# Optimization experiments

Measured on AMD Instinct MI355X. Metric: run time of the kernel, lower is better.

Reference implementation:

```python
import jax, jax.numpy as jnp
import numpy as np

N = 100000   # nodes
E = 1600000  # edges per relation (avg in-degree 16)
D = 128      # gcn_hidden (in_feat == out_feat)
R = 2        # relations: forward_edge, backward_edge


def setup_inputs() -> dict:
    key = jax.random.key(0)
    ks = jax.random.split(key, 8)
    x = jax.random.normal(ks[0], (N, D), dtype=jnp.float32)
    src_fwd = jax.random.randint(ks[1], (E,), 0, N, dtype=jnp.int32)
    dst_fwd = jax.random.randint(ks[2], (E,), 0, N, dtype=jnp.int32)
    src_bwd = jax.random.randint(ks[3], (E,), 0, N, dtype=jnp.int32)
    dst_bwd = jax.random.randint(ks[4], (E,), 0, N, dtype=jnp.int32)
    # xavier_uniform with relu gain sqrt(2)
    gain = np.sqrt(2.0)
    lim_rel = gain * np.sqrt(6.0 / (D + D))
    rel_weight = jax.random.uniform(ks[5], (R, D, D), minval=-lim_rel, maxval=lim_rel, dtype=jnp.float32)
    loop_weight = jax.random.uniform(ks[6], (D, D), minval=-lim_rel, maxval=lim_rel, dtype=jnp.float32)
    h_bias = jnp.zeros((D,), dtype=jnp.float32)
    return {
        'x': x,
        'src_fwd': src_fwd, 'dst_fwd': dst_fwd,
        'src_bwd': src_bwd, 'dst_bwd': dst_bwd,
        'rel_weight': rel_weight, 'loop_weight': loop_weight, 'h_bias': h_bias,
    }


def _rel_conv(x, src, dst, W):
    # dgl GraphConv(norm='right', weight per relation): scatter-sum src feats to
    # dst, divide by clamped in-degree, then matmul W (in_feat == out_feat so
    # order of matmul vs aggregation is mathematically equivalent).
    msg = x[src]                                            # [E, D] gather
    agg = jax.ops.segment_sum(msg, dst, num_segments=N)     # [N, D] scatter-add
    deg = jax.ops.segment_sum(jnp.ones((src.shape[0],), x.dtype), dst, num_segments=N)
    agg = agg / jnp.clip(deg, 1.0)[:, None]                 # right norm, deg clamp(min=1)
    return agg @ W                                          # [N, D]


def reference(x, src_fwd, dst_fwd, src_bwd, dst_bwd, rel_weight, loop_weight, h_bias):
    h = _rel_conv(x, src_fwd, dst_fwd, rel_weight[0])
    h = h + _rel_conv(x, src_bwd, dst_bwd, rel_weight[1])   # HeteroGraphConv sums per-relation results
    h = h + x @ loop_weight                                 # self loop
    h = h + h_bias                                          # bias
    h = jax.nn.relu(h)                                      # activation
    return h                                                # dropout is identity in eval
```

## Files before the change

### kernel.cpp

```cpp
#include <hip/hip_runtime.h>
#include <hip/hip_bf16.h>


#define DFEAT 128
#define CH2 16384
#define NBMAX 1600
#define CAP 3328

typedef __attribute__((ext_vector_type(8))) short short8v;
typedef __attribute__((ext_vector_type(4))) float float4v;

__global__ void convert_kernel(const float4* __restrict__ x4,
                               ushort4* __restrict__ xb4, int n4) {
    int i = blockIdx.x * blockDim.x + threadIdx.x;
    if (i >= n4) return;
    float4 v = x4[i];
    ushort4 o;
    o.x = __hip_bfloat16_raw(__float2bfloat16(v.x)).x;
    o.y = __hip_bfloat16_raw(__float2bfloat16(v.y)).x;
    o.z = __hip_bfloat16_raw(__float2bfloat16(v.z)).x;
    o.w = __hip_bfloat16_raw(__float2bfloat16(v.w)).x;
    xb4[i] = o;
}

__global__ void pack_b_kernel(const float* __restrict__ wrel,
                              const float* __restrict__ wloop,
                              unsigned short* __restrict__ wb) {
    int t = blockIdx.x * blockDim.x + threadIdx.x;
    if (t >= 12 * 8 * 64) return;
    int lane = t & 63;
    int kbase = (t >> 9) * 32 + (lane >> 4) * 8;
    int col = (((t >> 6) & 7) << 4) + (lane & 15);
    unsigned short tmp[8];
#pragma unroll
    for (int j = 0; j < 8; ++j) {
        int k = kbase + j;
        float v = (k < 256) ? wrel[k * DFEAT + col] : wloop[(k - 256) * DFEAT + col];
        tmp[j] = __hip_bfloat16_raw(__float2bfloat16(v)).x;
    }
    *(ushort4*)(wb + t * 8)     = make_ushort4(tmp[0], tmp[1], tmp[2], tmp[3]);
    *(ushort4*)(wb + t * 8 + 4) = make_ushort4(tmp[4], tmp[5], tmp[6], tmp[7]);
}

__global__ void zero_kernel(int* __restrict__ p, int n) {
    int i = blockIdx.x * blockDim.x + threadIdx.x;
    if (i < n) p[i] = 0;
}

__global__ __launch_bounds__(256) void hist_kernel(
        const int* __restrict__ dst0, const int* __restrict__ dst1,
        int* __restrict__ ghist, int N, int E, int NB) {
    __shared__ int h[NBMAX];
    int tid = threadIdx.x;
    for (int i = tid; i < NBMAX; i += 256) h[i] = 0;
    __syncthreads();
    int lo = blockIdx.x * CH2, hi = min(2 * E, lo + CH2);
    for (int i = lo + tid; i < hi; i += 256) {
        int r = (i >= E) ? 1 : 0;
        int e = i - r * E;
        int t = r ? dst1[e] : dst0[e];
        atomicAdd(&h[(r * N + t) >> 7], 1);
    }
    __syncthreads();
    for (int b = tid; b < NB; b += 256) {
        int c = h[b];
        if (c) atomicAdd(&ghist[b], c);
    }
}

__global__ __launch_bounds__(256) void scan_kernel(const int* __restrict__ ghist,
                                                   int* __restrict__ S,
                                                   int* __restrict__ cursor,
                                                   int n, int total) {
    __shared__ int psum[256];
    int t = threadIdx.x;
    int cs = (n + 255) / 256;
    int s = 0;
    for (int j = 0; j < cs; ++j) {
        int idx = t * cs + j;
        if (idx < n) s += ghist[idx];
    }
    psum[t] = s; __syncthreads();
    for (int off = 1; off < 256; off <<= 1) {
        int add = (t >= off) ? psum[t - off] : 0;
        __syncthreads();
        psum[t] += add;
        __syncthreads();
    }
    int run = psum[t] - s;
    for (int j = 0; j < cs; ++j) {
        int idx = t * cs + j;
        if (idx < n) { S[idx] = run; cursor[idx] = run; run += ghist[idx]; }
    }
    if (t == 0) S[n] = total;
}

__global__ __launch_bounds__(256) void bin_kernel(
        const int* __restrict__ src0, const int* __restrict__ dst0,
        const int* __restrict__ src1, const int* __restrict__ dst1,
        int* __restrict__ cursor, unsigned* __restrict__ binned, int N, int E) {
    __shared__ int cnt[NBMAX];
    __shared__ int base[NBMAX];
    int tid = threadIdx.x;
    for (int i = tid; i < NBMAX; i += 256) cnt[i] = 0;
    __syncthreads();
    int lo = blockIdx.x * CH2, hi = min(2 * E, lo + CH2);
    for (int i = lo + tid; i < hi; i += 256) {
        int r = (i >= E) ? 1 : 0;
        int e = i - r * E;
        int t = r ? dst1[e] : dst0[e];
        atomicAdd(&cnt[(r * N + t) >> 7], 1);
    }
    __syncthreads();
    for (int b = tid; b < NBMAX; b += 256) {
        int c = cnt[b];
        if (c) base[b] = atomicAdd(&cursor[b], c);
    }
    __syncthreads();
    for (int i = lo + tid; i < hi; i += 256) {
        int r = (i >= E) ? 1 : 0;
        int e = i - r * E;
        int s = r ? src1[e] : src0[e];
        int t = r ? dst1[e] : dst0[e];
        int p = r * N + t;
        int slot = atomicAdd(&base[p >> 7], 1);
        binned[slot] = ((unsigned)(p & 127) << 17) | (unsigned)s;
    }
}

__global__ __launch_bounds__(256) void agg_kernel(
        const uint2* __restrict__ xb2,
        const unsigned* __restrict__ binned,
        const int* __restrict__ S,
        unsigned short* __restrict__ aggb, int M) {
    __shared__ unsigned ebuf[CAP];
    __shared__ int cnt[128], cur[128], rs[128], sh[128];
    int tid = threadIdx.x;
    int b = blockIdx.x;
    int estart = S[b], eend = S[b + 1];
    int total = eend - estart;
    int P0 = b << 7;
    int hw = tid >> 5, lane = tid & 31;

    if (total <= CAP) {
        if (tid < 128) cnt[tid] = 0;
        __syncthreads();
        for (int i = estart + tid; i < eend; i += 256)
            atomicAdd(&cnt[binned[i] >> 17], 1);
        __syncthreads();
        if (tid < 128) sh[tid] = cnt[tid];
        __syncthreads();
        for (int off = 1; off < 128; off <<= 1) {
            int add = (tid < 128 && tid >= off) ? sh[tid - off] : 0;
            __syncthreads();
            if (tid < 128) sh[tid] += add;
            __syncthreads();
        }
        if (tid < 128) { rs[tid] = sh[tid] - cnt[tid]; cur[tid] = sh[tid] - cnt[tid]; }
        __syncthreads();
        for (int i = estart + tid; i < eend; i += 256) {
            unsigned v = binned[i];
            int slot = atomicAdd(&cur[v >> 17], 1);
            ebuf[slot] = v;
        }
        __syncthreads();

        for (int pi = 0; pi < 16; ++pi) {
            int pl = hw * 16 + pi;
            int s0 = rs[pl], c = cnt[pl];
            float a0 = 0.f, a1 = 0.f, a2 = 0.f, a3 = 0.f;
            int e = 0;
            for (; e + 4 <= c; e += 4) {
                int sA = ebuf[s0 + e] & 0x1FFFF;
                int sB = ebuf[s0 + e + 1] & 0x1FFFF;
                int sC = ebuf[s0 + e + 2] & 0x1FFFF;
                int sD = ebuf[s0 + e + 3] & 0x1FFFF;
                uint2 gA = xb2[(long long)sA * 32 + lane];
                uint2 gB = xb2[(long long)sB * 32 + lane];
                uint2 gC = xb2[(long long)sC * 32 + lane];
                uint2 gD = xb2[(long long)sD * 32 + lane];
                a0 += __uint_as_float(gA.x << 16) + __uint_as_float(gB.x << 16)
                    + __uint_as_float(gC.x << 16) + __uint_as_float(gD.x << 16);
                a1 += __uint_as_float(gA.x & 0xffff0000u) + __uint_as_float(gB.x & 0xffff0000u)
                    + __uint_as_float(gC.x & 0xffff0000u) + __uint_as_float(gD.x & 0xffff0000u);
                a2 += __uint_as_float(gA.y << 16) + __uint_as_float(gB.y << 16)
                    + __uint_as_float(gC.y << 16) + __uint_as_float(gD.y << 16);
                a3 += __uint_as_float(gA.y & 0xffff0000u) + __uint_as_float(gB.y & 0xffff0000u)
                    + __uint_as_float(gC.y & 0xffff0000u) + __uint_as_float(gD.y & 0xffff0000u);
            }
            for (; e < c; ++e) {
                int s = ebuf[s0 + e] & 0x1FFFF;
                uint2 g = xb2[(long long)s * 32 + lane];
                a0 += __uint_as_float(g.x << 16);
                a1 += __uint_as_float(g.x & 0xffff0000u);
                a2 += __uint_as_float(g.y << 16);
                a3 += __uint_as_float(g.y & 0xffff0000u);
            }
            int pg = P0 + pl;
            if (pg < M) {
                float inv = 1.0f / (float)max(c, 1);
                ushort4 w;
                w.x = __hip_bfloat16_raw(__float2bfloat16(a0 * inv)).x;
                w.y = __hip_bfloat16_raw(__float2bfloat16(a1 * inv)).x;
                w.z = __hip_bfloat16_raw(__float2bfloat16(a2 * inv)).x;
                w.w = __hip_bfloat16_raw(__float2bfloat16(a3 * inv)).x;
                *(ushort4*)(aggb + (long long)pg * DFEAT + 4 * lane) = w;
            }
        }
    } else {
        for (int pi = 0; pi < 16; ++pi) {
            int pl = hw * 16 + pi;
            float a0 = 0.f, a1 = 0.f, a2 = 0.f, a3 = 0.f;
            int c = 0;
            for (int i = estart; i < eend; ++i) {
                unsigned v = binned[i];
                if ((int)(v >> 17) == pl) {
                    ++c;
                    uint2 g = xb2[(long long)(v & 0x1FFFF) * 32 + lane];
                    a0 += __uint_as_float(g.x << 16);
                    a1 += __uint_as_float(g.x & 0xffff0000u);
                    a2 += __uint_as_float(g.y << 16);
                    a3 += __uint_as_float(g.y & 0xffff0000u);
                }
            }
            int pg = P0 + pl;
            if (pg < M) {
                float inv = 1.0f / (float)max(c, 1);
                ushort4 w;
                w.x = __hip_bfloat16_raw(__float2bfloat16(a0 * inv)).x;
                w.y = __hip_bfloat16_raw(__float2bfloat16(a1 * inv)).x;
                w.z = __hip_bfloat16_raw(__float2bfloat16(a2 * inv)).x;
                w.w = __hip_bfloat16_raw(__float2bfloat16(a3 * inv)).x;
                *(ushort4*)(aggb + (long long)pg * DFEAT + 4 * lane) = w;
            }
        }
    }
}

__global__ __launch_bounds__(256) void mfma_gemm_kernel(
        const unsigned short* __restrict__ aggb,
        const unsigned short* __restrict__ xb,
        const unsigned short* __restrict__ wb,
        const float* __restrict__ bias,
        float* __restrict__ out, int N) {
    int tid = threadIdx.x;
    int wv = tid >> 6, lane = tid & 63;
    int R0 = blockIdx.x * 128 + wv * 32;
    int mrow = lane & 15, quad = lane >> 4;

    float4v acc[2][8];
#pragma unroll
    for (int rt = 0; rt < 2; ++rt)
#pragma unroll
        for (int ct = 0; ct < 8; ++ct) acc[rt][ct] = (float4v){0.f, 0.f, 0.f, 0.f};

    int n0 = min(R0 + mrow, N - 1);
    int n1 = min(R0 + 16 + mrow, N - 1);

#pragma unroll
    for (int kc = 0; kc < 12; ++kc) {
        int off = (kc & 3) * 32 + quad * 8;
        const unsigned short* s0;
        const unsigned short* s1;
        if (kc < 4)      { s0 = aggb + (size_t)n0 * DFEAT;       s1 = aggb + (size_t)n1 * DFEAT; }
        else if (kc < 8) { s0 = aggb + (size_t)(N + n0) * DFEAT; s1 = aggb + (size_t)(N + n1) * DFEAT; }
        else             { s0 = xb + (size_t)n0 * DFEAT;         s1 = xb + (size_t)n1 * DFEAT; }
        short8v a0 = *(const short8v*)(s0 + off);
        short8v a1 = *(const short8v*)(s1 + off);
#pragma unroll
        for (int ct = 0; ct < 8; ++ct) {
            short8v bfr = *(const short8v*)(wb + (((kc * 8 + ct) << 6) + lane) * 8);
            acc[0][ct] = __builtin_amdgcn_mfma_f32_16x16x32_bf16(a0, bfr, acc[0][ct], 0, 0, 0);
            acc[1][ct] = __builtin_amdgcn_mfma_f32_16x16x32_bf16(a1, bfr, acc[1][ct], 0, 0, 0);
        }
    }

#pragma unroll
    for (int ct = 0; ct < 8; ++ct) {
        int col = ct * 16 + mrow;
        float bv = bias[col];
#pragma unroll
        for (int rt = 0; rt < 2; ++rt) {
#pragma unroll
            for (int i = 0; i < 4; ++i) {
                int row = R0 + rt * 16 + quad * 4 + i;
                if (row < N)
                    out[(size_t)row * DFEAT + col] = fmaxf(acc[rt][ct][i] + bv, 0.f);
            }
        }
    }
}

extern "C" void kernel_launch(void* const* d_in, const int* in_sizes, int n_in,
                              void* d_out, int out_size, void* d_ws, size_t ws_size,
                              hipStream_t stream) {
    const float* x      = (const float*)d_in[0];
    const int* src_fwd  = (const int*)d_in[1];
    const int* dst_fwd  = (const int*)d_in[2];
    const int* src_bwd  = (const int*)d_in[3];
    const int* dst_bwd  = (const int*)d_in[4];
    const float* wrel   = (const float*)d_in[5];
    const float* wloop  = (const float*)d_in[6];
    const float* hbias  = (const float*)d_in[7];
    float* out          = (float*)d_out;

    int N = in_sizes[0] / DFEAT;
    int E = in_sizes[1];
    int M = 2 * N;
    int TE = 2 * E;
    int NB = (M + 127) / 128;

    unsigned short* wb   = (unsigned short*)d_ws;
    unsigned* binned     = (unsigned*)(wb + 12 * 8 * 64 * 8);
    unsigned short* xb   = (unsigned short*)(binned + (size_t)TE);
    unsigned short* aggb = xb + (size_t)N * DFEAT;
    int* ghist           = (int*)(aggb + (size_t)M * DFEAT);
    int* S               = ghist + NB;
    int* cursor          = S + NB + 1;

    int n4 = N * (DFEAT / 4);
    convert_kernel<<<(n4 + 255) / 256, 256, 0, stream>>>(
        (const float4*)x, (ushort4*)xb, n4);

    pack_b_kernel<<<24, 256, 0, stream>>>(wrel, wloop, wb);

    zero_kernel<<<(NB + 255) / 256, 256, 0, stream>>>(ghist, NB);

    int nblk = (TE + CH2 - 1) / CH2;
    hist_kernel<<<nblk, 256, 0, stream>>>(dst_fwd, dst_bwd, ghist, N, E, NB);

    scan_kernel<<<1, 256, 0, stream>>>(ghist, S, cursor, NB, TE);

    bin_kernel<<<nblk, 256, 0, stream>>>(
        src_fwd, dst_fwd, src_bwd, dst_bwd, cursor, binned, N, E);

    agg_kernel<<<NB, 256, 0, stream>>>((const uint2*)xb, binned, S, aggb, M);

    mfma_gemm_kernel<<<(N + 127) / 128, 256, 0, stream>>>(
        aggb, xb, wb, hbias, out, N);
}
```

Measured before the change: 401.0 us.

## Halve aggregation bin size, fuse prep kernels, deepen gather unroll

Node bins shrink from 128 to 64 destination rows, which doubles the number of aggregation blocks and the bin histogram size, and the shared-memory edge buffer capacity drops to match. The bin kernel uses smaller edge chunks so more blocks run, and the separate convert, weight-pack and zero kernels become one prep kernel to cut launches. The gather loop now issues 8 independent row loads per iteration instead of 4, for more memory-level parallelism. The tradeoffs are more global cursor atomics and a higher chance that a bin overflows into the slow fallback path, since the buffer now holds 1792 edges against about 1024 expected.

```diff
diff --git a/kernel.cpp b/kernel.cpp
--- a/kernel.cpp
+++ b/kernel.cpp
@@ -3,48 +3,52 @@
 
 
 #define DFEAT 128
-#define CH2 16384
-#define NBMAX 1600
-#define CAP 3328
+#define CHH 16384
+#define CHB 8192
+#define NBMAX 3200
+#define CAP 1792
 
 typedef __attribute__((ext_vector_type(8))) short short8v;
 typedef __attribute__((ext_vector_type(4))) float float4v;
 
-__global__ void convert_kernel(const float4* __restrict__ x4,
-                               ushort4* __restrict__ xb4, int n4) {
-    int i = blockIdx.x * blockDim.x + threadIdx.x;
-    if (i >= n4) return;
-    float4 v = x4[i];
-    ushort4 o;
-    o.x = __hip_bfloat16_raw(__float2bfloat16(v.x)).x;
-    o.y = __hip_bfloat16_raw(__float2bfloat16(v.y)).x;
-    o.z = __hip_bfloat16_raw(__float2bfloat16(v.z)).x;
-    o.w = __hip_bfloat16_raw(__float2bfloat16(v.w)).x;
-    xb4[i] = o;
-}
-
-__global__ void pack_b_kernel(const float* __restrict__ wrel,
-                              const float* __restrict__ wloop,
-                              unsigned short* __restrict__ wb) {
-    int t = blockIdx.x * blockDim.x + threadIdx.x;
-    if (t >= 12 * 8 * 64) return;
-    int lane = t & 63;
-    int kbase = (t >> 9) * 32 + (lane >> 4) * 8;
-    int col = (((t >> 6) & 7) << 4) + (lane & 15);
-    unsigned short tmp[8];
-#pragma unroll
-    for (int j = 0; j < 8; ++j) {
-        int k = kbase + j;
-        float v = (k < 256) ? wrel[k * DFEAT + col] : wloop[(k - 256) * DFEAT + col];
-        tmp[j] = __hip_bfloat16_raw(__float2bfloat16(v)).x;
-    }
-    *(ushort4*)(wb + t * 8)     = make_ushort4(tmp[0], tmp[1], tmp[2], tmp[3]);
-    *(ushort4*)(wb + t * 8 + 4) = make_ushort4(tmp[4], tmp[5], tmp[6], tmp[7]);
-}
-
-__global__ void zero_kernel(int* __restrict__ p, int n) {
-    int i = blockIdx.x * blockDim.x + threadIdx.x;
-    if (i < n) p[i] = 0;
+__global__ __launch_bounds__(256) void prep_kernel(
+        const float4* __restrict__ x4, ushort4* __restrict__ xb4, int n4,
+        const float* __restrict__ wrel, const float* __restrict__ wloop,
+        unsigned short* __restrict__ wb,
+        int* __restrict__ ghist, int NB, int zb) {
+    int blk = blockIdx.x, tid = threadIdx.x;
+    if (blk < zb) {
+        int i = blk * 256 + tid;
+        if (i < NB) ghist[i] = 0;
+    } else if (blk < zb + 24) {
+        int t = (blk - zb) * 256 + tid;
+        if (t < 12 * 8 * 64) {
+            int lane = t & 63;
+            int kbase = (t >> 9) * 32 + (lane >> 4) * 8;
+            int col = (((t >> 6) & 7) << 4) + (lane & 15);
+            unsigned short tmp[8];
+#pragma unroll
+            for (int j = 0; j < 8; ++j) {
+                int k = kbase + j;
+                float v = (k < 256) ? wrel[k * DFEAT + col]
+                                    : wloop[(k - 256) * DFEAT + col];
+                tmp[j] = __hip_bfloat16_raw(__float2bfloat16(v)).x;
+            }
+            *(ushort4*)(wb + t * 8)     = make_ushort4(tmp[0], tmp[1], tmp[2], tmp[3]);
+            *(ushort4*)(wb + t * 8 + 4) = make_ushort4(tmp[4], tmp[5], tmp[6], tmp[7]);
+        }
+    } else {
+        int i = (blk - zb - 24) * 256 + tid;
+        if (i < n4) {
+            float4 v = x4[i];
+            ushort4 o;
+            o.x = __hip_bfloat16_raw(__float2bfloat16(v.x)).x;
+            o.y = __hip_bfloat16_raw(__float2bfloat16(v.y)).x;
+            o.z = __hip_bfloat16_raw(__float2bfloat16(v.z)).x;
+            o.w = __hip_bfloat16_raw(__float2bfloat16(v.w)).x;
+            xb4[i] = o;
+        }
+    }
 }
 
 __global__ __launch_bounds__(256) void hist_kernel(
@@ -54,12 +58,12 @@
     int tid = threadIdx.x;
     for (int i = tid; i < NBMAX; i += 256) h[i] = 0;
     __syncthreads();
-    int lo = blockIdx.x * CH2, hi = min(2 * E, lo + CH2);
+    int lo = blockIdx.x * CHH, hi = min(2 * E, lo + CHH);
     for (int i = lo + tid; i < hi; i += 256) {
         int r = (i >= E) ? 1 : 0;
         int e = i - r * E;
         int t = r ? dst1[e] : dst0[e];
-        atomicAdd(&h[(r * N + t) >> 7], 1);
+        atomicAdd(&h[(r * N + t) >> 6], 1);
     }
     __syncthreads();
     for (int b = tid; b < NB; b += 256) {
@@ -104,12 +108,12 @@
     int tid = threadIdx.x;
     for (int i = tid; i < NBMAX; i += 256) cnt[i] = 0;
     __syncthreads();
-    int lo = blockIdx.x * CH2, hi = min(2 * E, lo + CH2);
+    int lo = blockIdx.x * CHB, hi = min(2 * E, lo + CHB);
     for (int i = lo + tid; i < hi; i += 256) {
         int r = (i >= E) ? 1 : 0;
         int e = i - r * E;
         int t = r ? dst1[e] : dst0[e];
-        atomicAdd(&cnt[(r * N + t) >> 7], 1);
+        atomicAdd(&cnt[(r * N + t) >> 6], 1);
     }
     __syncthreads();
     for (int b = tid; b < NBMAX; b += 256) {
@@ -123,8 +127,8 @@
         int s = r ? src1[e] : src0[e];
         int t = r ? dst1[e] : dst0[e];
         int p = r * N + t;
-        int slot = atomicAdd(&base[p >> 7], 1);
-        binned[slot] = ((unsigned)(p & 127) << 17) | (unsigned)s;
+        int slot = atomicAdd(&base[p >> 6], 1);
+        binned[slot] = ((unsigned)(p & 63) << 17) | (unsigned)s;
     }
 }
 
@@ -134,29 +138,29 @@
         const int* __restrict__ S,
         unsigned short* __restrict__ aggb, int M) {
     __shared__ unsigned ebuf[CAP];
-    __shared__ int cnt[128], cur[128], rs[128], sh[128];
+    __shared__ int cnt[64], cur[64], rs[64], sh[64];
     int tid = threadIdx.x;
     int b = blockIdx.x;
     int estart = S[b], eend = S[b + 1];
     int total = eend - estart;
-    int P0 = b << 7;
+    int P0 = b << 6;
     int hw = tid >> 5, lane = tid & 31;
 
     if (total <= CAP) {
-        if (tid < 128) cnt[tid] = 0;
+        if (tid < 64) cnt[tid] = 0;
         __syncthreads();
         for (int i = estart + tid; i < eend; i += 256)
             atomicAdd(&cnt[binned[i] >> 17], 1);
         __syncthreads();
-        if (tid < 128) sh[tid] = cnt[tid];
-        __syncthreads();
-        for (int off = 1; off < 128; off <<= 1) {
-            int add = (tid < 128 && tid >= off) ? sh[tid - off] : 0;
+        if (tid < 64) sh[tid] = cnt[tid];
+        __syncthreads();
+        for (int off = 1; off < 64; off <<= 1) {
+            int add = (tid < 64 && tid >= off) ? sh[tid - off] : 0;
             __syncthreads();
-            if (tid < 128) sh[tid] += add;
+            if (tid < 64) sh[tid] += add;
             __syncthreads();
         }
-        if (tid < 128) { rs[tid] = sh[tid] - cnt[tid]; cur[tid] = sh[tid] - cnt[tid]; }
+        if (tid < 64) { rs[tid] = sh[tid] - cnt[tid]; cur[tid] = sh[tid] - cnt[tid]; }
         __syncthreads();
         for (int i = estart + tid; i < eend; i += 256) {
             unsigned v = binned[i];
@@ -165,28 +169,26 @@
         }
         __syncthreads();
 
-        for (int pi = 0; pi < 16; ++pi) {
-            int pl = hw * 16 + pi;
+#pragma unroll
+        for (int pi = 0; pi < 8; ++pi) {
+            int pl = hw * 8 + pi;
             int s0 = rs[pl], c = cnt[pl];
             float a0 = 0.f, a1 = 0.f, a2 = 0.f, a3 = 0.f;
             int e = 0;
-            for (; e + 4 <= c; e += 4) {
-                int sA = ebuf[s0 + e] & 0x1FFFF;
-                int sB = ebuf[s0 + e + 1] & 0x1FFFF;
-                int sC = ebuf[s0 + e + 2] & 0x1FFFF;
-                int sD = ebuf[s0 + e + 3] & 0x1FFFF;
-                uint2 gA = xb2[(long long)sA * 32 + lane];
-                uint2 gB = xb2[(long long)sB * 32 + lane];
-                uint2 gC = xb2[(long long)sC * 32 + lane];
-                uint2 gD = xb2[(long long)sD * 32 + lane];
-                a0 += __uint_as_float(gA.x << 16) + __uint_as_float(gB.x << 16)
-                    + __uint_as_float(gC.x << 16) + __uint_as_float(gD.x << 16);
-                a1 += __uint_as_float(gA.x & 0xffff0000u) + __uint_as_float(gB.x & 0xffff0000u)
-                    + __uint_as_float(gC.x & 0xffff0000u) + __uint_as_float(gD.x & 0xffff0000u);
-                a2 += __uint_as_float(gA.y << 16) + __uint_as_float(gB.y << 16)
-                    + __uint_as_float(gC.y << 16) + __uint_as_float(gD.y << 16);
-                a3 += __uint_as_float(gA.y & 0xffff0000u) + __uint_as_float(gB.y & 0xffff0000u)
-                    + __uint_as_float(gC.y & 0xffff0000u) + __uint_as_float(gD.y & 0xffff0000u);
+            for (; e + 8 <= c; e += 8) {
+                uint2 g[8];
+#pragma unroll
+                for (int j = 0; j < 8; ++j) {
+                    int s = ebuf[s0 + e + j] & 0x1FFFF;
+                    g[j] = xb2[(long long)s * 32 + lane];
+                }
+#pragma unroll
+                for (int j = 0; j < 8; ++j) {
+                    a0 += __uint_as_float(g[j].x << 16);
+                    a1 += __uint_as_float(g[j].x & 0xffff0000u);
+                    a2 += __uint_as_float(g[j].y << 16);
+                    a3 += __uint_as_float(g[j].y & 0xffff0000u);
+                }
             }
             for (; e < c; ++e) {
                 int s = ebuf[s0 + e] & 0x1FFFF;
@@ -208,8 +210,9 @@
             }
         }
     } else {
-        for (int pi = 0; pi < 16; ++pi) {
-            int pl = hw * 16 + pi;
+#pragma unroll
+        for (int pi = 0; pi < 8; ++pi) {
+            int pl = hw * 8 + pi;
             float a0 = 0.f, a1 = 0.f, a2 = 0.f, a3 = 0.f;
             int c = 0;
             for (int i = estart; i < eend; ++i) {
@@ -308,7 +311,7 @@
     int E = in_sizes[1];
     int M = 2 * N;
     int TE = 2 * E;
-    int NB = (M + 127) / 128;
+    int NB = (M + 63) / 64;
 
     unsigned short* wb   = (unsigned short*)d_ws;
     unsigned* binned     = (unsigned*)(wb + 12 * 8 * 64 * 8);
@@ -319,19 +322,18 @@
     int* cursor          = S + NB + 1;
 
     int n4 = N * (DFEAT / 4);
-    convert_kernel<<<(n4 + 255) / 256, 256, 0, stream>>>(
-        (const float4*)x, (ushort4*)xb, n4);
-
-    pack_b_kernel<<<24, 256, 0, stream>>>(wrel, wloop, wb);
-
-    zero_kernel<<<(NB + 255) / 256, 256, 0, stream>>>(ghist, NB);
-
-    int nblk = (TE + CH2 - 1) / CH2;
-    hist_kernel<<<nblk, 256, 0, stream>>>(dst_fwd, dst_bwd, ghist, N, E, NB);
+    int zb = (NB + 255) / 256;
+    int prep_blocks = zb + 24 + (n4 + 255) / 256;
+    prep_kernel<<<prep_blocks, 256, 0, stream>>>(
+        (const float4*)x, (ushort4*)xb, n4, wrel, wloop, wb, ghist, NB, zb);
+
+    int hblk = (TE + CHH - 1) / CHH;
+    hist_kernel<<<hblk, 256, 0, stream>>>(dst_fwd, dst_bwd, ghist, N, E, NB);
 
     scan_kernel<<<1, 256, 0, stream>>>(ghist, S, cursor, NB, TE);
 
-    bin_kernel<<<nblk, 256, 0, stream>>>(
+    int bblk = (TE + CHB - 1) / CHB;
+    bin_kernel<<<bblk, 256, 0, stream>>>(
         src_fwd, dst_fwd, src_bwd, dst_bwd, cursor, binned, N, E);
 
     agg_kernel<<<NB, 256, 0, stream>>>((const uint2*)xb, binned, S, aggb, M);
```

Result: no change. 401.3 us (+0.1%).
